# Performance work log

Measured on AMD Instinct MI355X. Metric: run time of the kernel, lower is better.

## Reference

```python
import jax, jax.numpy as jnp
import numpy as np

B, S, E, H, FF = 2, 2048, 768, 12, 3072
D = E // H
EPS = 1e-5


def setup_inputs() -> dict:
    key = jax.random.key(0)
    ks = jax.random.split(key, 12)
    sc = lambda n: 1.0 / np.sqrt(n)
    return {
        "x": jax.random.normal(ks[0], (B, S, E), jnp.float32),
        "wq": jax.random.normal(ks[1], (E, E), jnp.float32) * sc(E),
        "wk": jax.random.normal(ks[2], (E, E), jnp.float32) * sc(E),
        "wv": jax.random.normal(ks[3], (E, E), jnp.float32) * sc(E),
        "wo": jax.random.normal(ks[4], (E, E), jnp.float32) * sc(E),
        "bo": jax.random.normal(ks[5], (E,), jnp.float32) * 0.02,
        "w1": jax.random.normal(ks[6], (FF, E), jnp.float32) * sc(E),
        "b1": jax.random.normal(ks[7], (FF,), jnp.float32) * 0.02,
        "w2": jax.random.normal(ks[8], (E, FF), jnp.float32) * sc(FF),
        "b2": jax.random.normal(ks[9], (E,), jnp.float32) * 0.02,
        "gamma": jnp.ones((E,), jnp.float32),
        "beta": jnp.zeros((E,), jnp.float32),
    }


def _layernorm(x, g, b):
    mu = jnp.mean(x, axis=-1, keepdims=True)
    var = jnp.mean(jnp.square(x - mu), axis=-1, keepdims=True)
    return (x - mu) * jax.lax.rsqrt(var + EPS) * g + b


def reference(x, wq, wk, wv, wo, bo, w1, b1, w2, b2, gamma, beta):
    res = x
    xn = _layernorm(x, gamma, beta)
    # Q/K/V projections (torch Linear: y = x @ W.T), split into heads
    q = (xn @ wq.T).reshape(B, S, H, D)
    k = (xn @ wk.T).reshape(B, S, H, D)
    v = (xn @ wv.T).reshape(B, S, H, D)
    scale = jnp.sqrt(jnp.float32(D))
    scores = jnp.einsum("bqhd,bkhd->bhqk", q, k) / scale  # [B,H,S,S]
    causal = jnp.tril(jnp.ones((S, S), bool))
    scores = jnp.where(causal, scores, -jnp.inf)
    w = jax.nn.softmax(scores, axis=-1)
    attn = jnp.einsum("bhqk,bkhd->bqhd", w, v).reshape(B, S, E)
    attn = attn @ wo.T + bo
    res = res + attn
    y = _layernorm(res, gamma, beta)  # NOTE: same LayerNorm params reused (as in source)
    h = jax.nn.gelu(y @ w1.T + b1, approximate=False)  # nn.GELU default is exact erf
    ffn = h @ w2.T + b2
    return res + ffn
```

## Files before the change

kernel.cpp:

```cpp
#include <hip/hip_runtime.h>
#include <hip/hip_bf16.h>
#include <math.h>

typedef __bf16 bf16_8 __attribute__((ext_vector_type(8)));
typedef __bf16 bf16_4 __attribute__((ext_vector_type(4)));
typedef float f32x4 __attribute__((ext_vector_type(4)));

#define AS1 __attribute__((address_space(1)))
#define AS3 __attribute__((address_space(3)))

#define SCL_Q 0.18033688011112042f

__global__ __launch_bounds__(256) void ln_kernel(
    const float* __restrict__ x, const float* __restrict__ g,
    const float* __restrict__ b, __hip_bfloat16* __restrict__ out, int cols) {
  const int row = blockIdx.x;
  const int t = threadIdx.x;
  float loc[3];
  float s = 0.f, s2 = 0.f;
#pragma unroll
  for (int i = 0; i < 3; ++i) {
    float v = x[(size_t)row * cols + t + i * 256];
    loc[i] = v;
    s += v;
    s2 += v * v;
  }
#pragma unroll
  for (int off = 32; off; off >>= 1) {
    s += __shfl_down(s, off);
    s2 += __shfl_down(s2, off);
  }
  __shared__ float red[2][4];
  const int lane = t & 63, w = t >> 6;
  if (lane == 0) {
    red[0][w] = s;
    red[1][w] = s2;
  }
  __syncthreads();
  s = red[0][0] + red[0][1] + red[0][2] + red[0][3];
  s2 = red[1][0] + red[1][1] + red[1][2] + red[1][3];
  const float mu = s / cols;
  const float var = s2 / cols - mu * mu;
  const float rs = rsqrtf(var + 1e-5f);
  __hip_bfloat16* orow = out + (size_t)row * cols;
#pragma unroll
  for (int i = 0; i < 3; ++i) {
    int c = t + i * 256;
    orow[c] = __hip_bfloat16((loc[i] - mu) * rs * g[c] + b[c]);
  }
}

__global__ __launch_bounds__(256) void reduce_ln(
    const float* __restrict__ x, const float* __restrict__ part, int nz,
    const float* __restrict__ bias, const float* __restrict__ g,
    const float* __restrict__ b, float* __restrict__ res,
    __hip_bfloat16* __restrict__ yout) {
  const int row = blockIdx.x;
  const int t = threadIdx.x;
  const size_t zstride = (size_t)4096 * 768;
  float loc[3];
  float s = 0.f, s2 = 0.f;
#pragma unroll
  for (int i = 0; i < 3; ++i) {
    const int c = t + i * 256;
    const size_t off = (size_t)row * 768 + c;
    float v = x[off] + bias[c];
    for (int z = 0; z < nz; ++z) v += part[(size_t)z * zstride + off];
    res[off] = v;
    loc[i] = v;
    s += v;
    s2 += v * v;
  }
#pragma unroll
  for (int off = 32; off; off >>= 1) {
    s += __shfl_down(s, off);
    s2 += __shfl_down(s2, off);
  }
  __shared__ float red[2][4];
  const int lane = t & 63, w = t >> 6;
  if (lane == 0) {
    red[0][w] = s;
    red[1][w] = s2;
  }
  __syncthreads();
  s = red[0][0] + red[0][1] + red[0][2] + red[0][3];
  s2 = red[1][0] + red[1][1] + red[1][2] + red[1][3];
  const float mu = s / 768.f;
  const float var = s2 / 768.f - mu * mu;
  const float rs = rsqrtf(var + 1e-5f);
#pragma unroll
  for (int i = 0; i < 3; ++i) {
    const int c = t + i * 256;
    yout[(size_t)row * 768 + c] = __hip_bfloat16((loc[i] - mu) * rs * g[c] + b[c]);
  }
}

__global__ __launch_bounds__(256) void reduce_out(
    const float* __restrict__ part, int nz, const float* __restrict__ bias,
    float* __restrict__ res) {
  const int row = blockIdx.x;
  const int t = threadIdx.x;
  const size_t zstride = (size_t)4096 * 768;
#pragma unroll
  for (int i = 0; i < 3; ++i) {
    const int c = t + i * 256;
    const size_t off = (size_t)row * 768 + c;
    float v = res[off] + bias[c];
    for (int z = 0; z < nz; ++z) v += part[(size_t)z * zstride + off];
    res[off] = v;
  }
}

__global__ __launch_bounds__(256) void cvt_multi(
    const float* __restrict__ sa, const float* __restrict__ sb,
    const float* __restrict__ sc, const float* __restrict__ sd,
    __hip_bfloat16* __restrict__ da, __hip_bfloat16* __restrict__ db,
    __hip_bfloat16* __restrict__ dc, __hip_bfloat16* __restrict__ dd) {
  const float* src;
  __hip_bfloat16* dst;
  if (blockIdx.y == 0) { src = sa; dst = da; }
  else if (blockIdx.y == 1) { src = sb; dst = db; }
  else if (blockIdx.y == 2) { src = sc; dst = dc; }
  else { src = sd; dst = dd; }
  const size_t i = ((size_t)blockIdx.x * 256 + threadIdx.x) * 4;
  float4 f = *(const float4*)(src + i);
  bf16_4 o;
  o[0] = (__bf16)f.x; o[1] = (__bf16)f.y; o[2] = (__bf16)f.z; o[3] = (__bf16)f.w;
  *(bf16_4*)((__bf16*)dst + i) = o;
}

__global__ __launch_bounds__(256) void cvt_all(
    const float* __restrict__ wq, const float* __restrict__ wk,
    const float* __restrict__ wv, const float* __restrict__ wo,
    const float* __restrict__ w1, const float* __restrict__ w2,
    __hip_bfloat16* __restrict__ dA, __hip_bfloat16* __restrict__ dF) {
  const size_t EE = 589824, EF = 2359296;
  int bid = blockIdx.x;
  const float* src;
  __hip_bfloat16* dst;
  size_t off;
  if (bid < 2304) {
    const int m = bid / 576;
    off = (size_t)(bid - m * 576) * 1024;
    src = (m == 0) ? wq : (m == 1) ? wk : (m == 2) ? wv : wo;
    dst = dA + (size_t)m * EE;
  } else {
    bid -= 2304;
    const int m = bid / 2304;
    off = (size_t)(bid - m * 2304) * 1024;
    src = m ? w2 : w1;
    dst = dF + (size_t)m * EF;
  }
  const size_t i = off + (size_t)threadIdx.x * 4;
  float4 f = *(const float4*)(src + i);
  bf16_4 o;
  o[0] = (__bf16)f.x; o[1] = (__bf16)f.y; o[2] = (__bf16)f.z; o[3] = (__bf16)f.w;
  *(bf16_4*)((__bf16*)dst + i) = o;
}

__global__ __launch_bounds__(256) void transpose_v(
    const __hip_bfloat16* __restrict__ v, __hip_bfloat16* __restrict__ vt,
    int* __restrict__ ctr) {
  const int S = 2048, E = 768, H = 12;
  if (blockIdx.x == 0 && blockIdx.y == 0 && threadIdx.x == 0) *ctr = 0;
  const int s0 = blockIdx.x * 64;
  const int bh = blockIdx.y;
  const int b = bh / H, h = bh - b * H;
  __shared__ __align__(16) __bf16 T[64 * 72];
  const int tid = threadIdx.x;
#pragma unroll
  for (int u = 0; u < 2; ++u) {
    int i = tid + u * 256;
    int sr = i >> 3, c = i & 7;
    *(bf16_8*)(&T[sr * 72 + c * 8]) =
        *(const bf16_8*)(v + ((size_t)b * S + s0 + sr) * E + h * 64 + c * 8);
  }
  __syncthreads();
#pragma unroll
  for (int u = 0; u < 2; ++u) {
    int i = tid + u * 256;
    int dr = i >> 3, kc = i & 7;
    bf16_8 o;
#pragma unroll
    for (int e = 0; e < 8; ++e) {
      int k = 32 * (kc >> 2) + 16 * (e >> 2) + 4 * (kc & 3) + (e & 3);
      o[e] = T[k * 72 + dr];
    }
    *(bf16_8*)(vt + ((size_t)bh * 64 + dr) * S + s0 + kc * 8) = o;
  }
}

template <int MODE, bool BF32>
__global__ __launch_bounds__(256) void gemm_bt(
    const __hip_bfloat16* __restrict__ A, const void* __restrict__ Bx,
    const float* __restrict__ bias, void* __restrict__ out,
    int M, int N, int K, int lda, int ldb, int ldout) {
  constexpr int BM = 128, BN = 128, BK = 64;
  constexpr int LDBP = BF32 ? 72 : BK;
  __shared__ __align__(16) __bf16 As[BM * BK];
  __shared__ __align__(16) __bf16 Bs[BN * LDBP];
  const int tid = threadIdx.x;
  const int m0 = blockIdx.y * BM;
  const int n0 = blockIdx.x * BN;
  const int wave = tid >> 6;
  const int lane = tid & 63;
  const int quad = lane >> 4;
  const int l16 = lane & 15;
  const int wm = (wave & 1) * 64;
  const int wn = (wave >> 1) * 64;

  int kbase = 0, kcnt = K;
  if constexpr (MODE == 2 || MODE == 3) {
    kcnt = K / gridDim.z;
    kbase = blockIdx.z * kcnt;
  }

  const int srow = lane >> 3;
  const int scol = ((lane & 7) ^ (srow & 7)) * 8;
  const __hip_bfloat16* Ap = A + (size_t)(m0 + wave * 8 + srow) * lda + kbase + scol;
  const __hip_bfloat16* Bpb = nullptr;
  const float* Bpf = nullptr;
  if constexpr (BF32)
    Bpf = (const float*)Bx;
  else
    Bpb = (const __hip_bfloat16*)Bx + (size_t)(n0 + wave * 8 + srow) * ldb + kbase + scol;

  f32x4 acc[4][4] = {};

  for (int k0 = 0; k0 < kcnt; k0 += BK) {
    __syncthreads();
#pragma unroll
    for (int u = 0; u < 4; ++u) {
      __builtin_amdgcn_global_load_lds(
          (const AS1 void*)(Ap + (size_t)(u * 32) * lda + k0),
          (AS3 void*)(&As[(u * 32 + wave * 8) * BK]), 16, 0, 0);
      if constexpr (!BF32)
        __builtin_amdgcn_global_load_lds(
            (const AS1 void*)(Bpb + (size_t)(u * 32) * ldb + k0),
            (AS3 void*)(&Bs[(u * 32 + wave * 8) * BK]), 16, 0, 0);
    }
    if constexpr (BF32) {
#pragma unroll
      for (int u = 0; u < 4; ++u) {
        int c = u * 256 + tid;
        int row = c >> 3, kc = c & 7;
        const float* src = Bpf + (size_t)(n0 + row) * ldb + kbase + k0 + kc * 8;
        float4 f0 = *(const float4*)src;
        float4 f1 = *(const float4*)(src + 4);
        bf16_8 bv;
        bv[0] = (__bf16)f0.x; bv[1] = (__bf16)f0.y; bv[2] = (__bf16)f0.z; bv[3] = (__bf16)f0.w;
        bv[4] = (__bf16)f1.x; bv[5] = (__bf16)f1.y; bv[6] = (__bf16)f1.z; bv[7] = (__bf16)f1.w;
        *(bf16_8*)(&Bs[row * LDBP + kc * 8]) = bv;
      }
    }
    __syncthreads();
#pragma unroll
    for (int kk = 0; kk < 2; ++kk) {
      bf16_8 af[4], bfr[4];
#pragma unroll
      for (int i = 0; i < 4; ++i)
        af[i] = *(const bf16_8*)(
            &As[(wm + i * 16 + l16) * BK + (((kk * 4 + quad) ^ (l16 & 7)) * 8)]);
#pragma unroll
      for (int j = 0; j < 4; ++j) {
        if constexpr (BF32)
          bfr[j] = *(const bf16_8*)(&Bs[(wn + j * 16 + l16) * LDBP + kk * 32 + quad * 8]);
        else
          bfr[j] = *(const bf16_8*)(
              &Bs[(wn + j * 16 + l16) * BK + (((kk * 4 + quad) ^ (l16 & 7)) * 8)]);
      }
#pragma unroll
      for (int i = 0; i < 4; ++i)
#pragma unroll
        for (int j = 0; j < 4; ++j)
          acc[i][j] =
              __builtin_amdgcn_mfma_f32_16x16x32_bf16(af[i], bfr[j], acc[i][j], 0, 0, 0);
    }
  }

#pragma unroll
  for (int i = 0; i < 4; ++i) {
#pragma unroll
    for (int j = 0; j < 4; ++j) {
#pragma unroll
      for (int r = 0; r < 4; ++r) {
        const int row = m0 + wm + i * 16 + quad * 4 + r;
        const int col = n0 + wn + j * 16 + l16;
        const float v = acc[i][j][r];
        if constexpr (MODE == 0) {
          const int tsel = n0 / 768;
          const size_t idx = ((size_t)tsel * M + row) * 768 + (col - tsel * 768);
          const float vs = (tsel == 0) ? v * SCL_Q : v;
          ((__hip_bfloat16*)out)[idx] = __hip_bfloat16(vs);
        } else if constexpr (MODE == 1) {
          float tt = v + bias[col];
          float gl = 0.5f * tt * (1.0f + erff(tt * 0.70710678118654752f));
          ((__hip_bfloat16*)out)[(size_t)row * ldout + col] = __hip_bfloat16(gl);
        } else if constexpr (MODE == 2) {
          float add = v + ((blockIdx.z == 0 && bias) ? bias[col] : 0.f);
          atomicAdd((float*)out + (size_t)row * 768 + col, add);
        } else {
          ((float*)out)[(size_t)blockIdx.z * M * 768 + (size_t)row * 768 + col] = v;
        }
      }
    }
  }
}

__global__ void zero_ctr(int* __restrict__ c) {
  if (threadIdx.x == 0) *c = 0;
}

#define ALDP 72
__device__ __constant__ signed char UQ[48] = {
    31, 31, 30, 15, 30, 29, 29, 28, 14, 28, 27, 27, 26, 13, 26, 25,
    25, 24, 12, 24, 23, 23, 22, 11, 22, 21, 21, 20, 10, 20, 19, 19,
    18, 9, 18, 17, 17, 16, 8, 16, 7, 6, 5, 4, 3, 2, 1, 0};
__device__ __constant__ signed char UP[48] = {
    0, 1, 1, 2, 0, 0, 1, 1, 2, 0, 0, 1, 1, 2, 0, 0,
    1, 1, 2, 0, 0, 1, 1, 2, 0, 0, 1, 1, 2, 0, 0, 1,
    1, 2, 0, 0, 1, 1, 2, 0, 2, 2, 2, 2, 2, 2, 2, 2};

template <bool PRE_T, bool SPLIT>
__global__ __launch_bounds__(256) void attn_mfma(
    const __hip_bfloat16* __restrict__ qb, const __hip_bfloat16* __restrict__ kb,
    const __hip_bfloat16* __restrict__ vb, __hip_bfloat16* __restrict__ ob,
    float* __restrict__ po, float* __restrict__ pml, int* __restrict__ ctr) {
  const int S = 2048, H = 12, E = 768;
  const int tid = threadIdx.x;
  const int wave = tid >> 6;
  const int lane = tid & 63;
  const int quad = lane >> 4;
  const int l16 = lane & 15;

  __shared__ __align__(16) __bf16 Ks[64 * 64];
  __shared__ __align__(16) __bf16 Vt[2][64 * 64];
  __shared__ int task;
  __bf16* ep = &Vt[0][0] + wave * 16 * ALDP;

  const int srow8 = lane >> 3;
  const int csrc = ((lane & 7) ^ srow8) * 8;
  const int NTASK = SPLIT ? 24 * 48 : 24 * 32;

  for (;;) {
    if (tid == 0) task = atomicAdd(ctr, 1);
    __syncthreads();
    const int t = task;
    if (t >= NTASK) return;
    int qblk, part, bh;
    if constexpr (SPLIT) {
      const int unit = t / 24;
      bh = t - unit * 24;
      qblk = UQ[unit];
      part = UP[unit];
    } else {
      qblk = 31 - (t / 24);
      bh = t - (t / 24) * 24;
      part = 2;
    }
    const int b = bh / H, h = bh - b * H;
    const int q0 = qblk * 64;
    const int qw = q0 + wave * 16;
    const size_t base = (size_t)b * S * E + (size_t)h * 64;
    const int mid = (qblk + 1) >> 1;
    const int kbgn = (part == 1) ? mid : 0;
    const int kend = (part == 0) ? mid : qblk + 1;

    auto STAGE_K = [&](int kts) {
      const int k0s = kts * 64;
#pragma unroll
      for (int u = 0; u < 2; ++u) {
        const int trow = wave * 16 + u * 8;
        __builtin_amdgcn_global_load_lds(
            (const AS1 void*)(kb + base + (size_t)(k0s + trow + srow8) * E + csrc),
            (AS3 void*)(&Ks[trow * 64]), 16, 0, 0);
      }
    };
    auto STAGE_V = [&](int kts, int buf) {
      const int k0s = kts * 64;
      if constexpr (PRE_T) {
#pragma unroll
        for (int u = 0; u < 2; ++u) {
          const int trow = wave * 16 + u * 8;
          __builtin_amdgcn_global_load_lds(
              (const AS1 void*)(vb + ((size_t)(bh * 64 + trow + srow8)) * S + k0s + csrc),
              (AS3 void*)(&Vt[buf][trow * 64]), 16, 0, 0);
        }
      } else {
#pragma unroll
        for (int u = 0; u < 2; ++u) {
          int i = tid + u * 256;
          int kr = i & 63, dq = i >> 6;
          bf16_8 vv = *(const bf16_8*)(vb + base + (size_t)(k0s + kr) * E + dq * 8);
          const int c = 32 * (kr >> 5) + 8 * ((kr >> 2) & 3) + 4 * ((kr >> 4) & 1) + (kr & 3);
#pragma unroll
          for (int j = 0; j < 8; ++j) {
            int drow = dq * 8 + j;
            Vt[buf][drow * 64 + (((c >> 3) ^ (drow & 7)) * 8) + (c & 7)] = vv[j];
          }
        }
      }
    };

    bf16_8 qf[2];
#pragma unroll
    for (int s = 0; s < 2; ++s)
      qf[s] = *(const bf16_8*)(qb + base + (size_t)(qw + l16) * E + s * 32 + quad * 8);

    f32x4 o[4] = {};
    float mq = -1e30f, lq = 0.f;

    STAGE_K(kbgn);
    STAGE_V(kbgn, 0);
    __syncthreads();
    int cur = 0;

    for (int kt = kbgn; kt < kend; ++kt) {
      const int k0 = kt * 64;

      f32x4 sc[4] = {};
      __builtin_amdgcn_s_setprio(1);
#pragma unroll
      for (int jj = 0; jj < 4; ++jj)
#pragma unroll
        for (int s = 0; s < 2; ++s) {
          bf16_8 kf = *(const bf16_8*)(
              &Ks[(jj * 16 + l16) * 64 + (((s * 4 + quad) ^ (l16 & 7)) * 8)]);
          sc[jj] = __builtin_amdgcn_mfma_f32_16x16x32_bf16(kf, qf[s], sc[jj], 0, 0, 0);
        }
      __builtin_amdgcn_s_setprio(0);

      __syncthreads();
      if (kt + 1 < kend) {
        STAGE_K(kt + 1);
        STAGE_V(kt + 1, cur ^ 1);
      }

      if (kt == qblk) {
#pragma unroll
        for (int jj = 0; jj < 4; ++jj)
#pragma unroll
          for (int r = 0; r < 4; ++r)
            if ((k0 + jj * 16 + quad * 4 + r) > (qw + l16)) sc[jj][r] = -1e30f;
      }
      float mj[4];
#pragma unroll
      for (int jj = 0; jj < 4; ++jj)
        mj[jj] = fmaxf(fmaxf(sc[jj][0], sc[jj][1]), fmaxf(sc[jj][2], sc[jj][3]));
      float pmax = fmaxf(fmaxf(mj[0], mj[1]), fmaxf(mj[2], mj[3]));
      pmax = fmaxf(pmax, __shfl_xor(pmax, 16));
      pmax = fmaxf(pmax, __shfl_xor(pmax, 32));
      if (!__all(pmax <= mq + 11.5f)) {
        const float mn = fmaxf(mq, pmax);
        const float corr = exp2f(mq - mn);
        mq = mn;
        lq *= corr;
#pragma unroll
        for (int nt2 = 0; nt2 < 4; ++nt2)
#pragma unroll
          for (int r = 0; r < 4; ++r) o[nt2][r] *= corr;
      }
      float sj[4];
#pragma unroll
      for (int jj = 0; jj < 4; ++jj) {
#pragma unroll
        for (int r = 0; r < 4; ++r) sc[jj][r] = exp2f(sc[jj][r] - mq);
        sj[jj] = (sc[jj][0] + sc[jj][1]) + (sc[jj][2] + sc[jj][3]);
      }
      float sum = (sj[0] + sj[1]) + (sj[2] + sj[3]);
      sum += __shfl_xor(sum, 16);
      sum += __shfl_xor(sum, 32);
      lq += sum;

      bf16_8 pf[2];
#pragma unroll
      for (int s = 0; s < 2; ++s)
#pragma unroll
        for (int r = 0; r < 4; ++r) {
          pf[s][r] = (__bf16)sc[2 * s][r];
          pf[s][4 + r] = (__bf16)sc[2 * s + 1][r];
        }

      __builtin_amdgcn_s_setprio(1);
#pragma unroll
      for (int s = 0; s < 2; ++s)
#pragma unroll
        for (int dt = 0; dt < 4; ++dt) {
          bf16_8 vf = *(const bf16_8*)(
              &Vt[cur][(dt * 16 + l16) * 64 + (((s * 4 + quad) ^ (l16 & 7)) * 8)]);
          o[dt] = __builtin_amdgcn_mfma_f32_16x16x32_bf16(vf, pf[s], o[dt], 0, 0, 0);
        }
      __builtin_amdgcn_s_setprio(0);

      __syncthreads();
      cur ^= 1;
    }

    if (SPLIT && part != 2) {
      const int cidx = bh * 16 + (qblk - 16);
      float* poT = po + (size_t)cidx * 8192 + part * 4096;
      const int ql = wave * 16 + l16;
#pragma unroll
      for (int dt = 0; dt < 4; ++dt)
#pragma unroll
        for (int r = 0; r < 4; ++r)
          poT[(dt * 16 + quad * 4 + r) * 64 + ql] = o[dt][r];
      if (quad == 0) {
        pml[(size_t)cidx * 256 + part * 128 + ql] = mq;
        pml[(size_t)cidx * 256 + part * 128 + 64 + ql] = lq;
      }
    } else {
      const float inv = 1.f / lq;
#pragma unroll
      for (int dt = 0; dt < 4; ++dt) {
        bf16_4 o4;
#pragma unroll
        for (int r = 0; r < 4; ++r) o4[r] = (__bf16)(o[dt][r] * inv);
        *(bf16_4*)(&ep[l16 * ALDP + dt * 16 + quad * 4]) = o4;
      }
#pragma unroll
      for (int u = 0; u < 2; ++u) {
        int j = lane + u * 64;
        int ql = j >> 3, ch = j & 7;
        bf16_8 ov = *(const bf16_8*)(&ep[ql * ALDP + ch * 8]);
        *(bf16_8*)(ob + base + (size_t)(qw + ql) * E + ch * 8) = ov;
      }
    }
  }
}

__global__ __launch_bounds__(256) void attn_combine(
    const float* __restrict__ po, const float* __restrict__ pml,
    __hip_bfloat16* __restrict__ ob) {
  const int S = 2048, H = 12, E = 768;
  const int cidx = blockIdx.x;
  const int bh = cidx >> 4;
  const int qblk = 16 + (cidx & 15);
  const int b = bh / H, h = bh - b * H;
  const int q0 = qblk * 64;
  const size_t base = (size_t)b * S * E + (size_t)h * 64;
  const float* P0 = po + (size_t)cidx * 8192;
  const float* P1 = P0 + 4096;
  const float* ML = pml + (size_t)cidx * 256;

  __shared__ float a1[64], a2[64], dn[64];
  __shared__ float T[64 * 65];
  const int t = threadIdx.x;
  if (t < 64) {
    const float m1 = ML[t], l1 = ML[64 + t];
    const float m2 = ML[128 + t], l2 = ML[192 + t];
    const float ms = fmaxf(m1, m2);
    const float e1 = exp2f(m1 - ms), e2 = exp2f(m2 - ms);
    a1[t] = e1;
    a2[t] = e2;
    dn[t] = 1.f / (e1 * l1 + e2 * l2);
  }
  __syncthreads();
  const int q = t & 63;
  const int w = t >> 6;
#pragma unroll
  for (int i = 0; i < 16; ++i) {
    const int d = w * 16 + i;
    T[q * 65 + d] = (a1[q] * P0[d * 64 + q] + a2[q] * P1[d * 64 + q]) * dn[q];
  }
  __syncthreads();
  const int c8 = t & 7;
  const int qr = t >> 3;
#pragma unroll
  for (int p = 0; p < 2; ++p) {
    const int qq = qr + p * 32;
    bf16_8 ov;
#pragma unroll
    for (int j = 0; j < 8; ++j) ov[j] = (__bf16)T[qq * 65 + c8 * 8 + j];
    *(bf16_8*)(ob + base + (size_t)(q0 + qq) * E + c8 * 8) = ov;
  }
}

extern "C" void kernel_launch(void* const* d_in, const int* in_sizes, int n_in,
                              void* d_out, int out_size, void* d_ws, size_t ws_size,
                              hipStream_t stream) {
  const int Bv = 2, S = 2048, E = 768, FF = 3072;
  const int M = Bv * S;
  const size_t ME = (size_t)M * E;
  const size_t EE = (size_t)E * E;
  const size_t EF = (size_t)E * FF;

  const float* x = (const float*)d_in[0];
  const float* wq = (const float*)d_in[1];
  const float* wk = (const float*)d_in[2];
  const float* wv = (const float*)d_in[3];
  const float* wo = (const float*)d_in[4];
  const float* bo = (const float*)d_in[5];
  const float* w1 = (const float*)d_in[6];
  const float* b1 = (const float*)d_in[7];
  const float* w2 = (const float*)d_in[8];
  const float* b2 = (const float*)d_in[9];
  const float* gamma = (const float*)d_in[10];
  const float* beta = (const float*)d_in[11];

  int* ctr = (int*)d_ws;
  __hip_bfloat16* slot = (__hip_bfloat16*)((char*)d_ws + 256);
  __hip_bfloat16* s0 = slot;
  __hip_bfloat16* s1 = slot + ME;
  __hip_bfloat16* s4 = slot + 4 * ME;
  __hip_bfloat16* s5 = slot + 5 * ME;
  float* pp = (float*)(slot + 5 * ME + 2 * EF);
  __hip_bfloat16* vt = (__hip_bfloat16*)pp;
  float* po = (float*)((char*)pp + ME * sizeof(__hip_bfloat16));
  float* pml = po + (size_t)384 * 8192;
  float* res = (float*)d_out;

  const size_t need_mid = 256 + (5 * ME + 2 * EF) * sizeof(__hip_bfloat16);
  const size_t need_full = need_mid + 4 * ME * sizeof(float);
  const bool full = ws_size >= need_full;
  const bool mid = ws_size >= need_mid;

  if (mid)
    cvt_all<<<6912, 256, 0, stream>>>(wq, wk, wv, wo, w1, w2, s4, s5);
  else
    cvt_multi<<<dim3(EE / 1024, 4), 256, 0, stream>>>(
        wq, wk, wv, wo, s4, s4 + EE, s4 + 2 * EE, s4 + 3 * EE);
  ln_kernel<<<M, 256, 0, stream>>>(x, gamma, beta, s0, E);
  gemm_bt<0, false><<<dim3(18, 32), 256, 0, stream>>>(s0, s4, nullptr, s1, M, 2304, E, E, E, 0);
  if (full) {
    transpose_v<<<dim3(32, 24), 256, 0, stream>>>(s1 + 2 * ME, vt, ctr);
    attn_mfma<true, true><<<1152, 256, 0, stream>>>(s1, s1 + ME, vt, s0, po, pml, ctr);
    attn_combine<<<384, 256, 0, stream>>>(po, pml, s0);
  } else {
    zero_ctr<<<1, 64, 0, stream>>>(ctr);
    attn_mfma<false, false><<<768, 256, 0, stream>>>(
        s1, s1 + ME, s1 + 2 * ME, s0, nullptr, nullptr, ctr);
  }

  if (full) {
    gemm_bt<3, false><<<dim3(6, 32, 4), 256, 0, stream>>>(
        s0, s4 + 3 * EE, nullptr, pp, M, E, E, E, E, 0);
    reduce_ln<<<M, 256, 0, stream>>>(x, pp, 4, bo, gamma, beta, res, s0);
    gemm_bt<1, false><<<dim3(24, 32), 256, 0, stream>>>(s0, s5, b1, s1, M, FF, E, E, E, FF);
    gemm_bt<3, false><<<dim3(6, 32, 4), 256, 0, stream>>>(
        s1, s5 + EF, nullptr, pp, M, E, FF, FF, FF, 0);
    reduce_out<<<M, 256, 0, stream>>>(pp, 4, b2, res);
  } else {
    hipMemcpyAsync(d_out, x, ME * sizeof(float), hipMemcpyDeviceToDevice, stream);
    gemm_bt<2, false><<<dim3(6, 32, 2), 256, 0, stream>>>(
        s0, s4 + 3 * EE, bo, res, M, E, E, E, E, 0);
    ln_kernel<<<M, 256, 0, stream>>>(res, gamma, beta, s0, E);
    if (mid) {
      gemm_bt<1, false><<<dim3(24, 32), 256, 0, stream>>>(s0, s5, b1, s1, M, FF, E, E, E, FF);
      gemm_bt<2, false><<<dim3(6, 32, 4), 256, 0, stream>>>(
          s1, s5 + EF, b2, res, M, E, FF, FF, FF, 0);
    } else {
      gemm_bt<1, true><<<dim3(24, 32), 256, 0, stream>>>(s0, w1, b1, s1, M, FF, E, E, E, FF);
      cvt_multi<<<dim3(EF / 1024, 1), 256, 0, stream>>>(
          w2, nullptr, nullptr, nullptr, s0, nullptr, nullptr, nullptr);
      gemm_bt<2, false><<<dim3(6, 32, 4), 256, 0, stream>>>(
          s1, s0, b2, res, M, E, FF, FF, FF, 0);
    }
  }
}
```

Baseline: 309.0 us.

## Split causal attention into fixed 8-tile KV chunks with multi-part combine

Replaces the two-way split of long query blocks with splitting into chunks of at most 8 KV tiles, for query blocks 8 and above, with up to four partials per block. The combine kernel is generalized to merge a variable number of partial (max, sum, output) sets. The persistent grid is enlarged to match the higher task count. The intent is better load balance and shorter tail latency in the causal attention kernel. The cost is more partial-output traffic to global memory and a heavier combine pass.

```diff
diff --git a/kernel.cpp b/kernel.cpp
--- a/kernel.cpp
+++ b/kernel.cpp
@@ -312,14 +312,18 @@
 }
 
 #define ALDP 72
-__device__ __constant__ signed char UQ[48] = {
-    31, 31, 30, 15, 30, 29, 29, 28, 14, 28, 27, 27, 26, 13, 26, 25,
-    25, 24, 12, 24, 23, 23, 22, 11, 22, 21, 21, 20, 10, 20, 19, 19,
-    18, 9, 18, 17, 17, 16, 8, 16, 7, 6, 5, 4, 3, 2, 1, 0};
-__device__ __constant__ signed char UP[48] = {
-    0, 1, 1, 2, 0, 0, 1, 1, 2, 0, 0, 1, 1, 2, 0, 0,
-    1, 1, 2, 0, 0, 1, 1, 2, 0, 0, 1, 1, 2, 0, 0, 1,
-    1, 2, 0, 0, 1, 1, 2, 0, 2, 2, 2, 2, 2, 2, 2, 2};
+__device__ __constant__ signed char UQ[80] = {
+    8, 9, 10, 11, 12, 13, 14, 15, 15, 16, 16, 17, 17, 18, 18, 19,
+    19, 20, 20, 21, 21, 22, 22, 23, 23, 23, 24, 24, 24, 25, 25, 25,
+    26, 26, 26, 27, 27, 27, 28, 28, 28, 29, 29, 29, 30, 30, 30, 31,
+    31, 31, 31, 7, 14, 22, 30, 6, 13, 21, 29, 5, 12, 20, 28, 4,
+    11, 19, 27, 3, 10, 18, 26, 2, 9, 17, 25, 1, 8, 16, 24, 0};
+__device__ __constant__ signed char UP[80] = {
+    0, 0, 0, 0, 0, 0, 0, 0, 1, 0, 1, 0, 1, 0, 1, 0,
+    1, 0, 1, 0, 1, 0, 1, 0, 1, 2, 0, 1, 2, 0, 1, 2,
+    0, 1, 2, 0, 1, 2, 0, 1, 2, 0, 1, 2, 0, 1, 2, 0,
+    1, 2, 3, 7, 1, 2, 3, 7, 1, 2, 3, 7, 1, 2, 3, 7,
+    1, 2, 3, 7, 1, 2, 3, 7, 1, 2, 3, 7, 1, 2, 3, 7};
 
 template <bool PRE_T, bool SPLIT>
 __global__ __launch_bounds__(256) void attn_mfma(
@@ -340,7 +344,7 @@
 
   const int srow8 = lane >> 3;
   const int csrc = ((lane & 7) ^ srow8) * 8;
-  const int NTASK = SPLIT ? 24 * 48 : 24 * 32;
+  const int NTASK = SPLIT ? 24 * 80 : 24 * 32;
 
   for (;;) {
     if (tid == 0) task = atomicAdd(ctr, 1);
@@ -356,15 +360,16 @@
     } else {
       qblk = 31 - (t / 24);
       bh = t - (t / 24) * 24;
-      part = 2;
+      part = 7;
     }
     const int b = bh / H, h = bh - b * H;
     const int q0 = qblk * 64;
     const int qw = q0 + wave * 16;
     const size_t base = (size_t)b * S * E + (size_t)h * 64;
-    const int mid = (qblk + 1) >> 1;
-    const int kbgn = (part == 1) ? mid : 0;
-    const int kend = (part == 0) ? mid : qblk + 1;
+    const bool prt = SPLIT && part != 7;
+    const int kbgn = prt ? part * 8 : 0;
+    int kend = qblk + 1;
+    if (prt && kbgn + 8 < kend) kend = kbgn + 8;
 
     auto STAGE_K = [&](int kts) {
       const int k0s = kts * 64;
@@ -496,9 +501,9 @@
       cur ^= 1;
     }
 
-    if (SPLIT && part != 2) {
-      const int cidx = bh * 16 + (qblk - 16);
-      float* poT = po + (size_t)cidx * 8192 + part * 4096;
+    if (prt) {
+      const int slot = bh * 24 + (qblk - 8);
+      float* poT = po + (size_t)slot * 16384 + part * 4096;
       const int ql = wave * 16 + l16;
 #pragma unroll
       for (int dt = 0; dt < 4; ++dt)
@@ -506,8 +511,8 @@
         for (int r = 0; r < 4; ++r)
           poT[(dt * 16 + quad * 4 + r) * 64 + ql] = o[dt][r];
       if (quad == 0) {
-        pml[(size_t)cidx * 256 + part * 128 + ql] = mq;
-        pml[(size_t)cidx * 256 + part * 128 + 64 + ql] = lq;
+        pml[(size_t)slot * 512 + part * 128 + ql] = mq;
+        pml[(size_t)slot * 512 + part * 128 + 64 + ql] = lq;
       }
     } else {
       const float inv = 1.f / lq;
@@ -534,26 +539,29 @@
     __hip_bfloat16* __restrict__ ob) {
   const int S = 2048, H = 12, E = 768;
   const int cidx = blockIdx.x;
-  const int bh = cidx >> 4;
-  const int qblk = 16 + (cidx & 15);
+  const int bh = cidx / 24;
+  const int qblk = 8 + (cidx - bh * 24);
+  const int np = qblk / 8 + 1;
   const int b = bh / H, h = bh - b * H;
   const int q0 = qblk * 64;
   const size_t base = (size_t)b * S * E + (size_t)h * 64;
-  const float* P0 = po + (size_t)cidx * 8192;
-  const float* P1 = P0 + 4096;
-  const float* ML = pml + (size_t)cidx * 256;
-
-  __shared__ float a1[64], a2[64], dn[64];
+  const float* PB = po + (size_t)cidx * 16384;
+  const float* ML = pml + (size_t)cidx * 512;
+
+  __shared__ float aw[4][64];
+  __shared__ float dn[64];
   __shared__ float T[64 * 65];
   const int t = threadIdx.x;
   if (t < 64) {
-    const float m1 = ML[t], l1 = ML[64 + t];
-    const float m2 = ML[128 + t], l2 = ML[192 + t];
-    const float ms = fmaxf(m1, m2);
-    const float e1 = exp2f(m1 - ms), e2 = exp2f(m2 - ms);
-    a1[t] = e1;
-    a2[t] = e2;
-    dn[t] = 1.f / (e1 * l1 + e2 * l2);
+    float ms = -1e30f;
+    for (int p = 0; p < np; ++p) ms = fmaxf(ms, ML[p * 128 + t]);
+    float den = 0.f;
+    for (int p = 0; p < np; ++p) {
+      const float e = exp2f(ML[p * 128 + t] - ms);
+      aw[p][t] = e;
+      den += e * ML[p * 128 + 64 + t];
+    }
+    dn[t] = 1.f / den;
   }
   __syncthreads();
   const int q = t & 63;
@@ -561,7 +569,9 @@
 #pragma unroll
   for (int i = 0; i < 16; ++i) {
     const int d = w * 16 + i;
-    T[q * 65 + d] = (a1[q] * P0[d * 64 + q] + a2[q] * P1[d * 64 + q]) * dn[q];
+    float acc = 0.f;
+    for (int p = 0; p < np; ++p) acc += aw[p][q] * PB[p * 4096 + d * 64 + q];
+    T[q * 65 + d] = acc * dn[q];
   }
   __syncthreads();
   const int c8 = t & 7;
@@ -607,7 +617,7 @@
   float* pp = (float*)(slot + 5 * ME + 2 * EF);
   __hip_bfloat16* vt = (__hip_bfloat16*)pp;
   float* po = (float*)((char*)pp + ME * sizeof(__hip_bfloat16));
-  float* pml = po + (size_t)384 * 8192;
+  float* pml = po + (size_t)576 * 16384;
   float* res = (float*)d_out;
 
   const size_t need_mid = 256 + (5 * ME + 2 * EF) * sizeof(__hip_bfloat16);
@@ -624,8 +634,8 @@
   gemm_bt<0, false><<<dim3(18, 32), 256, 0, stream>>>(s0, s4, nullptr, s1, M, 2304, E, E, E, 0);
   if (full) {
     transpose_v<<<dim3(32, 24), 256, 0, stream>>>(s1 + 2 * ME, vt, ctr);
-    attn_mfma<true, true><<<1152, 256, 0, stream>>>(s1, s1 + ME, vt, s0, po, pml, ctr);
-    attn_combine<<<384, 256, 0, stream>>>(po, pml, s0);
+    attn_mfma<true, true><<<1536, 256, 0, stream>>>(s1, s1 + ME, vt, s0, po, pml, ctr);
+    attn_combine<<<576, 256, 0, stream>>>(po, pml, s0);
   } else {
     zero_ctr<<<1, 64, 0, stream>>>(ctr);
     attn_mfma<false, false><<<768, 256, 0, stream>>>(
```

After: 339.6 us. 9.9% more time.

## Replace split-K output projection with 64x64-tile GEMM that fuses residual add

Applied to the files above, without the earlier changes.

The attention output projection previously ran as a split-K GEMM writing four fp32 partial buffers, followed by a kernel that summed them, added bias and residual, and applied LayerNorm. A new 64x64-tile MFMA GEMM now covers the full K=768 per block (768 blocks) and writes x + acc + bias straight into the residual buffer. The plain LayerNorm kernel then runs on it. This removes the partial-sum write/read traffic, at the cost of a separate LN pass that rereads res, and uses a smaller tile that gets less reuse per block.

```diff
diff --git a/kernel.cpp b/kernel.cpp
--- a/kernel.cpp
+++ b/kernel.cpp
@@ -47,51 +47,6 @@
   for (int i = 0; i < 3; ++i) {
     int c = t + i * 256;
     orow[c] = __hip_bfloat16((loc[i] - mu) * rs * g[c] + b[c]);
-  }
-}
-
-__global__ __launch_bounds__(256) void reduce_ln(
-    const float* __restrict__ x, const float* __restrict__ part, int nz,
-    const float* __restrict__ bias, const float* __restrict__ g,
-    const float* __restrict__ b, float* __restrict__ res,
-    __hip_bfloat16* __restrict__ yout) {
-  const int row = blockIdx.x;
-  const int t = threadIdx.x;
-  const size_t zstride = (size_t)4096 * 768;
-  float loc[3];
-  float s = 0.f, s2 = 0.f;
-#pragma unroll
-  for (int i = 0; i < 3; ++i) {
-    const int c = t + i * 256;
-    const size_t off = (size_t)row * 768 + c;
-    float v = x[off] + bias[c];
-    for (int z = 0; z < nz; ++z) v += part[(size_t)z * zstride + off];
-    res[off] = v;
-    loc[i] = v;
-    s += v;
-    s2 += v * v;
-  }
-#pragma unroll
-  for (int off = 32; off; off >>= 1) {
-    s += __shfl_down(s, off);
-    s2 += __shfl_down(s2, off);
-  }
-  __shared__ float red[2][4];
-  const int lane = t & 63, w = t >> 6;
-  if (lane == 0) {
-    red[0][w] = s;
-    red[1][w] = s2;
-  }
-  __syncthreads();
-  s = red[0][0] + red[0][1] + red[0][2] + red[0][3];
-  s2 = red[1][0] + red[1][1] + red[1][2] + red[1][3];
-  const float mu = s / 768.f;
-  const float var = s2 / 768.f - mu * mu;
-  const float rs = rsqrtf(var + 1e-5f);
-#pragma unroll
-  for (int i = 0; i < 3; ++i) {
-    const int c = t + i * 256;
-    yout[(size_t)row * 768 + c] = __hip_bfloat16((loc[i] - mu) * rs * g[c] + b[c]);
   }
 }
 
@@ -307,6 +262,77 @@
   }
 }
 
+__global__ __launch_bounds__(256) void gemm_proj64(
+    const __hip_bfloat16* __restrict__ A, const __hip_bfloat16* __restrict__ B,
+    const float* __restrict__ x, const float* __restrict__ bias,
+    float* __restrict__ res) {
+  constexpr int BK = 64;
+  const int K = 768;
+  __shared__ __align__(16) __bf16 As[64 * BK];
+  __shared__ __align__(16) __bf16 Bs[64 * BK];
+  const int tid = threadIdx.x;
+  const int m0 = blockIdx.y * 64;
+  const int n0 = blockIdx.x * 64;
+  const int wave = tid >> 6;
+  const int lane = tid & 63;
+  const int quad = lane >> 4;
+  const int l16 = lane & 15;
+  const int wm = (wave & 1) * 32;
+  const int wn = (wave >> 1) * 32;
+
+  const int srow = lane >> 3;
+  const int scol = ((lane & 7) ^ (srow & 7)) * 8;
+  const __hip_bfloat16* Ap = A + (size_t)(m0 + srow) * K + scol;
+  const __hip_bfloat16* Bp = B + (size_t)(n0 + srow) * K + scol;
+
+  f32x4 acc[2][2] = {};
+
+  for (int k0 = 0; k0 < K; k0 += BK) {
+    __syncthreads();
+#pragma unroll
+    for (int u = 0; u < 2; ++u) {
+      const int rr = u * 32 + wave * 8;
+      __builtin_amdgcn_global_load_lds(
+          (const AS1 void*)(Ap + (size_t)rr * K + k0),
+          (AS3 void*)(&As[rr * BK]), 16, 0, 0);
+      __builtin_amdgcn_global_load_lds(
+          (const AS1 void*)(Bp + (size_t)rr * K + k0),
+          (AS3 void*)(&Bs[rr * BK]), 16, 0, 0);
+    }
+    __syncthreads();
+#pragma unroll
+    for (int kk = 0; kk < 2; ++kk) {
+      bf16_8 af[2], bfr[2];
+#pragma unroll
+      for (int i = 0; i < 2; ++i)
+        af[i] = *(const bf16_8*)(
+            &As[(wm + i * 16 + l16) * BK + (((kk * 4 + quad) ^ (l16 & 7)) * 8)]);
+#pragma unroll
+      for (int j = 0; j < 2; ++j)
+        bfr[j] = *(const bf16_8*)(
+            &Bs[(wn + j * 16 + l16) * BK + (((kk * 4 + quad) ^ (l16 & 7)) * 8)]);
+#pragma unroll
+      for (int i = 0; i < 2; ++i)
+#pragma unroll
+        for (int j = 0; j < 2; ++j)
+          acc[i][j] =
+              __builtin_amdgcn_mfma_f32_16x16x32_bf16(af[i], bfr[j], acc[i][j], 0, 0, 0);
+    }
+  }
+
+#pragma unroll
+  for (int i = 0; i < 2; ++i)
+#pragma unroll
+    for (int j = 0; j < 2; ++j)
+#pragma unroll
+      for (int r = 0; r < 4; ++r) {
+        const int row = m0 + wm + i * 16 + quad * 4 + r;
+        const int col = n0 + wn + j * 16 + l16;
+        const size_t idx = (size_t)row * 768 + col;
+        res[idx] = x[idx] + acc[i][j][r] + bias[col];
+      }
+}
+
 __global__ void zero_ctr(int* __restrict__ c) {
   if (threadIdx.x == 0) *c = 0;
 }
@@ -633,9 +659,8 @@
   }
 
   if (full) {
-    gemm_bt<3, false><<<dim3(6, 32, 4), 256, 0, stream>>>(
-        s0, s4 + 3 * EE, nullptr, pp, M, E, E, E, E, 0);
-    reduce_ln<<<M, 256, 0, stream>>>(x, pp, 4, bo, gamma, beta, res, s0);
+    gemm_proj64<<<dim3(12, 64), 256, 0, stream>>>(s0, s4 + 3 * EE, x, bo, res);
+    ln_kernel<<<M, 256, 0, stream>>>(res, gamma, beta, s0, E);
     gemm_bt<1, false><<<dim3(24, 32), 256, 0, stream>>>(s0, s5, b1, s1, M, FF, E, E, E, FF);
     gemm_bt<3, false><<<dim3(6, 32, 4), 256, 0, stream>>>(
         s1, s5 + EF, nullptr, pp, M, E, FF, FF, FF, 0);
```

Measured after the change: 301.8 us. 2.3% less time.
